# Kernel optimization log

Measured on AMD Instinct MI355X. Metric: run time of the kernel, lower is better.

## Reference

```python
import jax, jax.numpy as jnp
import numpy as np

N, E, D_IN, D_OUT = 50000, 800000, 128, 128


def setup_inputs() -> dict:
    key = jax.random.key(0)
    ks = jax.random.split(key, 4)
    x = jax.random.normal(ks[0], (N, D_IN), jnp.float32)
    edge_index = jax.random.randint(ks[1], (2, E), 0, N)
    # GCNConv.lin weight (no bias in lin; bias added after aggregation)
    W = jax.random.normal(ks[2], (D_IN, D_OUT), jnp.float32) / np.sqrt(D_IN)
    b = jnp.zeros((D_OUT,), jnp.float32)
    # edge_weight_predictor: Linear(2*dim_in, 1)
    w_pred = jax.random.normal(ks[3], (2 * D_IN, 1), jnp.float32) / np.sqrt(2 * D_IN)
    b_pred = jnp.zeros((1,), jnp.float32)
    return {"x": x, "edge_index": edge_index, "W": W, "b": b,
            "w_pred": w_pred, "b_pred": b_pred}


def reference(x, edge_index, W, b, w_pred, b_pred):
    n = x.shape[0]
    src, tgt = edge_index[0], edge_index[1]

    # --- learned edge weights: gather, concat, linear, sigmoid ---
    eemb = jnp.concatenate([x[src], x[tgt]], axis=1)          # [E, 2D]
    ew = jax.nn.sigmoid(eemb @ w_pred + b_pred)[:, 0]         # [E]

    # --- GCNConv with edge_weight (PyG gcn_norm: add self-loops w=1) ---
    loop = jnp.arange(n)
    row = jnp.concatenate([src, loop])                        # message sources
    col = jnp.concatenate([tgt, loop])                        # aggregation targets
    w_full = jnp.concatenate([ew, jnp.ones((n,), ew.dtype)])

    deg = jax.ops.segment_sum(w_full, col, num_segments=n)    # weighted in-degree
    dis = jnp.where(deg > 0, jax.lax.rsqrt(deg), 0.0)         # deg^{-1/2}, inf->0
    norm = dis[row] * w_full * dis[col]                       # [E+N]

    xw = x @ W                                                # [N, D_OUT]
    msg = norm[:, None] * xw[row]                             # [E+N, D_OUT]
    out = jax.ops.segment_sum(msg, col, num_segments=n) + b   # [N, D_OUT]
    return out
```

## Files before the change

### kernel.cpp

```cpp
#include <hip/hip_runtime.h>
#include <math.h>

#define D 128
#define NC 16

typedef __attribute__((ext_vector_type(8))) short bf16x8;
typedef __attribute__((ext_vector_type(4))) float f32x4;

__device__ __forceinline__ unsigned int bf16_round(float f) {
  unsigned int u = __float_as_uint(f);
  return (u + 0x7fffu + ((u >> 16) & 1u)) >> 16;
}
__device__ __forceinline__ float bf_lo(unsigned int u) { return __uint_as_float(u << 16); }
__device__ __forceinline__ float bf_hi(unsigned int u) { return __uint_as_float(u & 0xffff0000u); }

__global__ __launch_bounds__(256) void k_pq(const float* __restrict__ x,
                                            const float* __restrict__ w_pred,
                                            float* __restrict__ p, float* __restrict__ q,
                                            unsigned int* __restrict__ xbh, int n) {
  int wid = (blockIdx.x * blockDim.x + threadIdx.x) >> 6;
  int lane = threadIdx.x & 63;
  if (wid >= n) return;
  float2 xv = ((const float2*)(x + (size_t)wid * D))[lane];
  xbh[(size_t)wid * 64 + lane] = bf16_round(xv.x) | (bf16_round(xv.y) << 16);
  float2 wp = ((const float2*)w_pred)[lane];
  float2 wq = ((const float2*)w_pred)[64 + lane];
  float pp = xv.x * wp.x + xv.y * wp.y;
  float qq = xv.x * wq.x + xv.y * wq.y;
#pragma unroll
  for (int off = 32; off > 0; off >>= 1) {
    pp += __shfl_down(pp, off);
    qq += __shfl_down(qq, off);
  }
  if (lane == 0) { p[wid] = pp; q[wid] = qq; }
}

__global__ __launch_bounds__(256) void k_wt(const float* __restrict__ W,
                                            unsigned short* __restrict__ wt) {
  int i = blockIdx.x * 256 + threadIdx.x;
  int col = i >> 7, k = i & 127;
  wt[col * 128 + k] = (unsigned short)bf16_round(W[k * 128 + col]);
}

__global__ __launch_bounds__(256) void k_hist(const int* __restrict__ tgt,
                                              int* __restrict__ rank,
                                              int* __restrict__ partial,
                                              int E, int n) {
  int e = blockIdx.x * blockDim.x + threadIdx.x;
  if (e >= E) return;
  int t = tgt[e];
  int c = (e >> 8) & (NC - 1);
  rank[e] = atomicAdd(&partial[c * n + t], 1);
}

__global__ __launch_bounds__(256) void k_scan1(const int* __restrict__ partial,
                                               int* __restrict__ rowptr,
                                               int* __restrict__ bsum, int n) {
  __shared__ int wsum[4];
  int base = blockIdx.x * 1024 + threadIdx.x * 4;
  int4 v = make_int4(0, 0, 0, 0);
  if (base + 3 < n) {
#pragma unroll
    for (int c = 0; c < NC; ++c) {
      int4 t = *(const int4*)(partial + (size_t)c * n + base);
      v.x += t.x; v.y += t.y; v.z += t.z; v.w += t.w;
    }
  } else {
#pragma unroll
    for (int c = 0; c < NC; ++c) {
      const int* pc = partial + (size_t)c * n;
      if (base + 0 < n) v.x += pc[base + 0];
      if (base + 1 < n) v.y += pc[base + 1];
      if (base + 2 < n) v.z += pc[base + 2];
      if (base + 3 < n) v.w += pc[base + 3];
    }
  }
  int s = v.x + v.y + v.z + v.w;
  int lane = threadIdx.x & 63;
  int wave = threadIdx.x >> 6;
  int incl = s;
#pragma unroll
  for (int off = 1; off < 64; off <<= 1) {
    int t = __shfl_up(incl, off);
    if (lane >= off) incl += t;
  }
  if (lane == 63) wsum[wave] = incl;
  __syncthreads();
  int woff = 0;
#pragma unroll
  for (int w = 0; w < 4; ++w) if (w < wave) woff += wsum[w];
  int excl = woff + incl - s;
  if (base + 0 < n) rowptr[base + 0] = excl;
  if (base + 1 < n) rowptr[base + 1] = excl + v.x;
  if (base + 2 < n) rowptr[base + 2] = excl + v.x + v.y;
  if (base + 3 < n) rowptr[base + 3] = excl + v.x + v.y + v.z;
  if (threadIdx.x == 255) bsum[blockIdx.x] = woff + incl;
}

__global__ __launch_bounds__(256) void k_cursors(int* __restrict__ rowptr,
                                                 const int* __restrict__ bsum,
                                                 const int* __restrict__ partial,
                                                 int* __restrict__ cursor,
                                                 int n, int E, int nb) {
  __shared__ int bpre_s[64];
  if (threadIdx.x < 64) {
    int lane = threadIdx.x;
    int v = (lane < nb) ? bsum[lane] : 0;
    int incl = v;
#pragma unroll
    for (int off = 1; off < 64; off <<= 1) {
      int t = __shfl_up(incl, off);
      if (lane >= off) incl += t;
    }
    bpre_s[lane] = incl - v;
  }
  __syncthreads();
  int t = blockIdx.x * blockDim.x + threadIdx.x;
  if (t < n) {
    int r = rowptr[t] + bpre_s[t >> 10];
    rowptr[t] = r;
#pragma unroll
    for (int c = 0; c < NC; ++c) {
      cursor[c * n + t] = r;
      r += partial[c * n + t];
    }
  }
  if (t == 0) rowptr[n] = E;
}

__global__ __launch_bounds__(256) void k_fill(const int* __restrict__ src,
                                              const int* __restrict__ tgt,
                                              const int* __restrict__ rank,
                                              const int* __restrict__ cursor,
                                              int* __restrict__ ecol, int E, int n) {
  int e = blockIdx.x * blockDim.x + threadIdx.x;
  if (e >= E) return;
  int t = tgt[e];
  int c = (e >> 8) & (NC - 1);
  int pos = cursor[c * n + t] + rank[e];
  ecol[pos] = src[e];
}

__global__ __launch_bounds__(256) void k_node(const int* __restrict__ rowptr,
                                              const int* __restrict__ ecol,
                                              const float* __restrict__ p,
                                              const float* __restrict__ q,
                                              const float* __restrict__ b_pred,
                                              float* __restrict__ ewt,
                                              float* __restrict__ dis, int n) {
  int wid = (blockIdx.x * blockDim.x + threadIdx.x) >> 6;
  int lane = threadIdx.x & 63;
  if (wid >= n) return;
  int beg = rowptr[wid], end = rowptr[wid + 1];
  float qt = q[wid] + b_pred[0];
  float sum = 0.0f;
  for (int j0 = beg; j0 < end; j0 += 64) {
    int j = j0 + lane;
    float w = 0.0f;
    if (j < end) {
      int s = ecol[j];
      float z = p[s] + qt;
      w = 1.0f / (1.0f + expf(-z));
      ewt[j] = w;
    }
    sum += w;
  }
#pragma unroll
  for (int off = 32; off > 0; off >>= 1) sum += __shfl_down(sum, off);
  if (lane == 0) {
    float d = 1.0f + sum;
    dis[wid] = (d > 0.0f) ? rsqrtf(d) : 0.0f;
  }
}

__global__ __launch_bounds__(256) void k_gemm_mfma(const short* __restrict__ xbh,
                                                   const short* __restrict__ wt,
                                                   const float* __restrict__ dis,
                                                   unsigned int* __restrict__ xwh, int n) {
  __shared__ float cbuf[4][16 * 128];
  int wave = threadIdx.x >> 6;
  int lane = threadIdx.x & 63;
  int row0 = blockIdx.x * 64 + wave * 16;
  int rA = lane & 15, quad = lane >> 4;

  f32x4 acc[8];
#pragma unroll
  for (int cb = 0; cb < 8; ++cb) acc[cb] = (f32x4){0.f, 0.f, 0.f, 0.f};

  const short* arow = xbh + (size_t)(row0 + rA) * 128 + quad * 8;
  bool arow_ok = (row0 + rA) < n;
#pragma unroll
  for (int kk = 0; kk < 4; ++kk) {
    bf16x8 a;
    if (arow_ok) a = *(const bf16x8*)(arow + kk * 32);
    else a = (bf16x8){0, 0, 0, 0, 0, 0, 0, 0};
#pragma unroll
    for (int cb = 0; cb < 8; ++cb) {
      bf16x8 bf = *(const bf16x8*)(wt + (size_t)(cb * 16 + rA) * 128 + kk * 32 + quad * 8);
      acc[cb] = __builtin_amdgcn_mfma_f32_16x16x32_bf16(a, bf, acc[cb], 0, 0, 0);
    }
  }

#pragma unroll
  for (int cb = 0; cb < 8; ++cb)
#pragma unroll
    for (int r = 0; r < 4; ++r)
      cbuf[wave][(quad * 4 + r) * 128 + cb * 16 + rA] = acc[cb][r];
  __syncthreads();

  int rr = lane >> 2;
  int ch = (lane & 3) * 32;
  int grow = row0 + rr;
  if (grow < n) {
    float dv = dis[grow];
    const float* cr = &cbuf[wave][rr * 128 + ch];
#pragma unroll
    for (int g = 0; g < 2; ++g) {
      uint4 o;
      o.x = bf16_round(cr[g * 16 + 0] * dv)  | (bf16_round(cr[g * 16 + 1] * dv) << 16);
      o.y = bf16_round(cr[g * 16 + 2] * dv)  | (bf16_round(cr[g * 16 + 3] * dv) << 16);
      o.z = bf16_round(cr[g * 16 + 4] * dv)  | (bf16_round(cr[g * 16 + 5] * dv) << 16);
      o.w = bf16_round(cr[g * 16 + 6] * dv)  | (bf16_round(cr[g * 16 + 7] * dv) << 16);
      uint4 o2;
      o2.x = bf16_round(cr[g * 16 + 8] * dv)  | (bf16_round(cr[g * 16 + 9] * dv) << 16);
      o2.y = bf16_round(cr[g * 16 + 10] * dv) | (bf16_round(cr[g * 16 + 11] * dv) << 16);
      o2.z = bf16_round(cr[g * 16 + 12] * dv) | (bf16_round(cr[g * 16 + 13] * dv) << 16);
      o2.w = bf16_round(cr[g * 16 + 14] * dv) | (bf16_round(cr[g * 16 + 15] * dv) << 16);
      *(uint4*)(xwh + (size_t)grow * 64 + (ch >> 1) + g * 8)     = o;
      *(uint4*)(xwh + (size_t)grow * 64 + (ch >> 1) + g * 8 + 4) = o2;
    }
  }
}

__global__ __launch_bounds__(256) void k_gather(const int* __restrict__ rowptr,
                                                const int* __restrict__ ecol,
                                                const float* __restrict__ ewt,
                                                const uint4* __restrict__ xwh4,
                                                const float* __restrict__ dis,
                                                const float* __restrict__ b,
                                                float* __restrict__ out, int n) {
  int wid = (blockIdx.x * blockDim.x + threadIdx.x) >> 6;
  int lane = threadIdx.x & 63;
  if (wid >= n) return;
  int cj = lane & 15;
  int rg = lane >> 4;
  int beg = rowptr[wid], end = rowptr[wid + 1];

  float acc[8];
  if (rg == 0) {
    uint4 v = xwh4[(size_t)wid * 16 + cj];
    acc[0] = bf_lo(v.x); acc[1] = bf_hi(v.x);
    acc[2] = bf_lo(v.y); acc[3] = bf_hi(v.y);
    acc[4] = bf_lo(v.z); acc[5] = bf_hi(v.z);
    acc[6] = bf_lo(v.w); acc[7] = bf_hi(v.w);
  } else {
#pragma unroll
    for (int i = 0; i < 8; ++i) acc[i] = 0.0f;
  }

  for (int j0 = beg; j0 < end; j0 += 64) {
    int m = end - j0; if (m > 64) m = 64;
    int sl = 0; float cl = 0.0f;
    if (lane < m) { sl = ecol[j0 + lane]; cl = ewt[j0 + lane]; }
    for (int k = 0; k < m; k += 4) {
      int idx = k + rg;
      int s = __shfl(sl, idx);
      float c = __shfl(cl, idx);
      if (idx >= m) { s = 0; c = 0.0f; }
      uint4 v = xwh4[(size_t)s * 16 + cj];
      acc[0] = fmaf(c, bf_lo(v.x), acc[0]);
      acc[1] = fmaf(c, bf_hi(v.x), acc[1]);
      acc[2] = fmaf(c, bf_lo(v.y), acc[2]);
      acc[3] = fmaf(c, bf_hi(v.y), acc[3]);
      acc[4] = fmaf(c, bf_lo(v.z), acc[4]);
      acc[5] = fmaf(c, bf_hi(v.z), acc[5]);
      acc[6] = fmaf(c, bf_lo(v.w), acc[6]);
      acc[7] = fmaf(c, bf_hi(v.w), acc[7]);
    }
  }

#pragma unroll
  for (int i = 0; i < 8; ++i) {
    acc[i] += __shfl_xor(acc[i], 16);
    acc[i] += __shfl_xor(acc[i], 32);
  }

  if (rg == 0) {
    float dt = dis[wid];
    float4 b0 = ((const float4*)b)[cj * 2];
    float4 b1 = ((const float4*)b)[cj * 2 + 1];
    float4 o0, o1;
    o0.x = fmaf(dt, acc[0], b0.x); o0.y = fmaf(dt, acc[1], b0.y);
    o0.z = fmaf(dt, acc[2], b0.z); o0.w = fmaf(dt, acc[3], b0.w);
    o1.x = fmaf(dt, acc[4], b1.x); o1.y = fmaf(dt, acc[5], b1.y);
    o1.z = fmaf(dt, acc[6], b1.z); o1.w = fmaf(dt, acc[7], b1.w);
    ((float4*)out)[(size_t)wid * 32 + cj * 2] = o0;
    ((float4*)out)[(size_t)wid * 32 + cj * 2 + 1] = o1;
  }
}

extern "C" void kernel_launch(void* const* d_in, const int* in_sizes, int n_in,
                              void* d_out, int out_size, void* d_ws, size_t ws_size,
                              hipStream_t stream) {
  const float* x      = (const float*)d_in[0];
  const int*   ei     = (const int*)d_in[1];
  const float* W      = (const float*)d_in[2];
  const float* b      = (const float*)d_in[3];
  const float* w_pred = (const float*)d_in[4];
  const float* b_pred = (const float*)d_in[5];

  int n = in_sizes[0] / D;
  int E = in_sizes[1] / 2;
  const int* src = ei;
  const int* tgt = ei + E;

  float* out = (float*)d_out;
  float* ws  = (float*)d_ws;
  unsigned int* xwh = (unsigned int*)ws;
  unsigned int* xbh = xwh + (size_t)n * 64;
  float* p       = (float*)(xbh + (size_t)n * 64);
  float* q       = p + n;
  float* dis     = q + n;
  float* ewt     = dis + n;
  int*   ecol    = (int*)(ewt + E);
  int*   rank    = ecol + E;
  int*   partial = rank + E;
  int*   cursor  = partial + (size_t)NC * n;
  int*   rowptr  = cursor + (size_t)NC * n;
  int*   bsum    = rowptr + n + 1;
  unsigned short* wt = (unsigned short*)(bsum + 64);

  int nb = (n + 1023) / 1024;

  (void)hipMemsetAsync(partial, 0, (size_t)NC * n * sizeof(int), stream);
  k_pq<<<(n + 3) / 4, 256, 0, stream>>>(x, w_pred, p, q, xbh, n);
  k_wt<<<64, 256, 0, stream>>>(W, wt);
  k_hist<<<(E + 255) / 256, 256, 0, stream>>>(tgt, rank, partial, E, n);
  k_scan1<<<nb, 256, 0, stream>>>(partial, rowptr, bsum, n);
  k_cursors<<<(n + 255) / 256, 256, 0, stream>>>(rowptr, bsum, partial, cursor, n, E, nb);
  k_fill<<<(E + 255) / 256, 256, 0, stream>>>(src, tgt, rank, cursor, ecol, E, n);
  k_node<<<(n + 3) / 4, 256, 0, stream>>>(rowptr, ecol, p, q, b_pred, ewt, dis, n);
  k_gemm_mfma<<<(n + 63) / 64, 256, 0, stream>>>((const short*)xbh, (const short*)wt, dis, xwh, n);
  k_gather<<<(n + 3) / 4, 256, 0, stream>>>(rowptr, ecol, ewt, (const uint4*)xwh, dis, b, out, n);
}
```

Baseline: 213.7 us.

## Fuse memset and weight transpose into k_pq; compute edge weights in fill

The partial-count memset and the W transpose/bf16 conversion are folded into the k_pq kernel, which removes two launches. The edge sigmoid weight is now computed per edge in k_fill and stored with the source index as an interleaved int2 (epair) in CSR order. The old k_node becomes a lighter k_dis that only sums those weights, and the gather reads a single int2 per edge instead of two arrays. The fill kernel now does random reads of p[s] and q[t], and its scattered stores grow to 8 bytes.

```diff
diff --git a/kernel.cpp b/kernel.cpp
--- a/kernel.cpp
+++ b/kernel.cpp
@@ -16,9 +16,20 @@
 
 __global__ __launch_bounds__(256) void k_pq(const float* __restrict__ x,
                                             const float* __restrict__ w_pred,
+                                            const float* __restrict__ W,
                                             float* __restrict__ p, float* __restrict__ q,
-                                            unsigned int* __restrict__ xbh, int n) {
-  int wid = (blockIdx.x * blockDim.x + threadIdx.x) >> 6;
+                                            unsigned int* __restrict__ xbh,
+                                            unsigned short* __restrict__ wt,
+                                            int* __restrict__ partial, int n) {
+  int tid = blockIdx.x * 256 + threadIdx.x;
+  int total = NC * n;
+  int gsz = gridDim.x * 256;
+  for (int i = tid; i < total; i += gsz) partial[i] = 0;
+  if (tid < 16384) {
+    int col = tid >> 7, k = tid & 127;
+    wt[col * 128 + k] = (unsigned short)bf16_round(W[k * 128 + col]);
+  }
+  int wid = tid >> 6;
   int lane = threadIdx.x & 63;
   if (wid >= n) return;
   float2 xv = ((const float2*)(x + (size_t)wid * D))[lane];
@@ -33,13 +44,6 @@
     qq += __shfl_down(qq, off);
   }
   if (lane == 0) { p[wid] = pp; q[wid] = qq; }
-}
-
-__global__ __launch_bounds__(256) void k_wt(const float* __restrict__ W,
-                                            unsigned short* __restrict__ wt) {
-  int i = blockIdx.x * 256 + threadIdx.x;
-  int col = i >> 7, k = i & 127;
-  wt[col * 128 + k] = (unsigned short)bf16_round(W[k * 128 + col]);
 }
 
 __global__ __launch_bounds__(256) void k_hist(const int* __restrict__ tgt,
@@ -132,39 +136,29 @@
                                               const int* __restrict__ tgt,
                                               const int* __restrict__ rank,
                                               const int* __restrict__ cursor,
-                                              int* __restrict__ ecol, int E, int n) {
-  int e = blockIdx.x * blockDim.x + threadIdx.x;
-  if (e >= E) return;
-  int t = tgt[e];
-  int c = (e >> 8) & (NC - 1);
-  int pos = cursor[c * n + t] + rank[e];
-  ecol[pos] = src[e];
-}
-
-__global__ __launch_bounds__(256) void k_node(const int* __restrict__ rowptr,
-                                              const int* __restrict__ ecol,
                                               const float* __restrict__ p,
                                               const float* __restrict__ q,
                                               const float* __restrict__ b_pred,
-                                              float* __restrict__ ewt,
-                                              float* __restrict__ dis, int n) {
+                                              int2* __restrict__ epair, int E, int n) {
+  int e = blockIdx.x * blockDim.x + threadIdx.x;
+  if (e >= E) return;
+  int s = src[e], t = tgt[e];
+  int c = (e >> 8) & (NC - 1);
+  int pos = cursor[c * n + t] + rank[e];
+  float z = p[s] + q[t] + b_pred[0];
+  float w = 1.0f / (1.0f + expf(-z));
+  epair[pos] = make_int2(s, __float_as_int(w));
+}
+
+__global__ __launch_bounds__(256) void k_dis(const int* __restrict__ rowptr,
+                                             const int2* __restrict__ epair,
+                                             float* __restrict__ dis, int n) {
   int wid = (blockIdx.x * blockDim.x + threadIdx.x) >> 6;
   int lane = threadIdx.x & 63;
   if (wid >= n) return;
   int beg = rowptr[wid], end = rowptr[wid + 1];
-  float qt = q[wid] + b_pred[0];
   float sum = 0.0f;
-  for (int j0 = beg; j0 < end; j0 += 64) {
-    int j = j0 + lane;
-    float w = 0.0f;
-    if (j < end) {
-      int s = ecol[j];
-      float z = p[s] + qt;
-      w = 1.0f / (1.0f + expf(-z));
-      ewt[j] = w;
-    }
-    sum += w;
-  }
+  for (int j = beg + lane; j < end; j += 64) sum += __int_as_float(epair[j].y);
 #pragma unroll
   for (int off = 32; off > 0; off >>= 1) sum += __shfl_down(sum, off);
   if (lane == 0) {
@@ -233,8 +227,7 @@
 }
 
 __global__ __launch_bounds__(256) void k_gather(const int* __restrict__ rowptr,
-                                                const int* __restrict__ ecol,
-                                                const float* __restrict__ ewt,
+                                                const int2* __restrict__ epair,
                                                 const uint4* __restrict__ xwh4,
                                                 const float* __restrict__ dis,
                                                 const float* __restrict__ b,
@@ -261,7 +254,10 @@
   for (int j0 = beg; j0 < end; j0 += 64) {
     int m = end - j0; if (m > 64) m = 64;
     int sl = 0; float cl = 0.0f;
-    if (lane < m) { sl = ecol[j0 + lane]; cl = ewt[j0 + lane]; }
+    if (lane < m) {
+      int2 pr = epair[j0 + lane];
+      sl = pr.x; cl = __int_as_float(pr.y);
+    }
     for (int k = 0; k < m; k += 4) {
       int idx = k + rg;
       int s = __shfl(sl, idx);
@@ -321,9 +317,8 @@
   float* p       = (float*)(xbh + (size_t)n * 64);
   float* q       = p + n;
   float* dis     = q + n;
-  float* ewt     = dis + n;
-  int*   ecol    = (int*)(ewt + E);
-  int*   rank    = ecol + E;
+  int2*  epair   = (int2*)(dis + n);
+  int*   rank    = (int*)(epair + E);
   int*   partial = rank + E;
   int*   cursor  = partial + (size_t)NC * n;
   int*   rowptr  = cursor + (size_t)NC * n;
@@ -332,14 +327,12 @@
 
   int nb = (n + 1023) / 1024;
 
-  (void)hipMemsetAsync(partial, 0, (size_t)NC * n * sizeof(int), stream);
-  k_pq<<<(n + 3) / 4, 256, 0, stream>>>(x, w_pred, p, q, xbh, n);
-  k_wt<<<64, 256, 0, stream>>>(W, wt);
+  k_pq<<<(n + 3) / 4, 256, 0, stream>>>(x, w_pred, W, p, q, xbh, wt, partial, n);
   k_hist<<<(E + 255) / 256, 256, 0, stream>>>(tgt, rank, partial, E, n);
   k_scan1<<<nb, 256, 0, stream>>>(partial, rowptr, bsum, n);
   k_cursors<<<(n + 255) / 256, 256, 0, stream>>>(rowptr, bsum, partial, cursor, n, E, nb);
-  k_fill<<<(E + 255) / 256, 256, 0, stream>>>(src, tgt, rank, cursor, ecol, E, n);
-  k_node<<<(n + 3) / 4, 256, 0, stream>>>(rowptr, ecol, p, q, b_pred, ewt, dis, n);
+  k_fill<<<(E + 255) / 256, 256, 0, stream>>>(src, tgt, rank, cursor, p, q, b_pred, epair, E, n);
+  k_dis<<<(n + 3) / 4, 256, 0, stream>>>(rowptr, epair, dis, n);
   k_gemm_mfma<<<(n + 63) / 64, 256, 0, stream>>>((const short*)xbh, (const short*)wt, dis, xwh, n);
-  k_gather<<<(n + 3) / 4, 256, 0, stream>>>(rowptr, ecol, ewt, (const uint4*)xwh, dis, b, out, n);
-}
+  k_gather<<<(n + 3) / 4, 256, 0, stream>>>(rowptr, epair, (const uint4*)xwh, dis, b, out, n);
+}
```

Measured after the change: 209.9 us. No clear change (-1.8%).
